# Kernel optimization log

Hardware: AMD Instinct MI355X
Metric: run time of the kernel (lower is better)

Reference implementation:

```python
import jax, jax.numpy as jnp
import numpy as np
from jax import lax

BATCH, SEQ_LEN, INPUT_DIM, OUTPUT_DIM = 64, 1000, 512, 512
KERNEL_WIDTH = 5  # context [-2, 2] with full_context=True -> range(-2, 3)


def setup_inputs() -> dict:
    key = jax.random.key(0)
    k1, k2, k3 = jax.random.split(key, 3)
    stdv = 1.0 / np.sqrt(INPUT_DIM)
    x = jax.random.normal(k1, (BATCH, SEQ_LEN, INPUT_DIM), dtype=jnp.float32)
    kernel = stdv * jax.random.normal(k2, (OUTPUT_DIM, INPUT_DIM, KERNEL_WIDTH), dtype=jnp.float32)
    bias = stdv * jax.random.normal(k3, (OUTPUT_DIM,), dtype=jnp.float32)
    return {"x": x, "kernel": kernel, "bias": bias}


def reference(x, kernel, bias):
    # x: [B, T, C_in] -> [B, C_in, T]
    xt = jnp.transpose(x, (0, 2, 1))
    # Contiguous full context == single VALID conv over time.
    # Original loop: for each valid step i, gather x[:, :, context+i] and conv1d,
    # which for context=range(-2,3) is exactly this strided convolution.
    out = lax.conv_general_dilated(
        xt, kernel,
        window_strides=(1,), padding="VALID",
        dimension_numbers=("NCH", "OIH", "NCH"),
    )  # [B, C_out, T - K + 1]
    out = out + bias[None, :, None]
    # ReLU then transpose back to [B, T_valid, C_out]
    return jnp.transpose(jax.nn.relu(out), (0, 2, 1))
```

## Files before the change

### kernel.cpp

```cpp
#include <hip/hip_runtime.h>
#include <hip/hip_bf16.h>


#define BATCH 64
#define SEQ   1000
#define CIN   512
#define COUT  512
#define TOUT  996
#define KTOT  2560
#define MTOT  63744
#define NKT   40
#define MT    498
#define NT    4
#define NWG   (MT*NT)

typedef __bf16 bf16x8 __attribute__((ext_vector_type(8)));
typedef float  f32x4  __attribute__((ext_vector_type(4)));

__device__ __forceinline__ void gload_lds16(const void* g, void* l) {
  __builtin_amdgcn_global_load_lds(
      (const __attribute__((address_space(1))) void*)g,
      (__attribute__((address_space(3))) void*)l, 16, 0, 0);
}

#define BAR()    __builtin_amdgcn_s_barrier()
#define VM12()   asm volatile("s_waitcnt vmcnt(12)" ::: "memory")
#define VM8()    asm volatile("s_waitcnt vmcnt(8)"  ::: "memory")
#define VM4()    asm volatile("s_waitcnt vmcnt(4)"  ::: "memory")
#define PRIO(x)  __builtin_amdgcn_s_setprio(x)
#define SCHED0() __builtin_amdgcn_sched_barrier(0)
#define MFMA(d, x, y) d = __builtin_amdgcn_mfma_f32_16x16x32_bf16(x, y, d, 0, 0, 0)

__global__ void cvt_x_kernel(const float* __restrict__ x, __bf16* __restrict__ xb, int n) {
  int i = (blockIdx.x * blockDim.x + threadIdx.x) * 8;
  if (i >= n) return;
  float4 f0 = *(const float4*)(x + i);
  float4 f1 = *(const float4*)(x + i + 4);
  bf16x8 v;
  v[0] = (__bf16)f0.x; v[1] = (__bf16)f0.y; v[2] = (__bf16)f0.z; v[3] = (__bf16)f0.w;
  v[4] = (__bf16)f1.x; v[5] = (__bf16)f1.y; v[6] = (__bf16)f1.z; v[7] = (__bf16)f1.w;
  *(bf16x8*)(xb + i) = v;
}

__global__ void cvt_w_kernel(const float* __restrict__ k, __bf16* __restrict__ wt) {
  int idx = blockIdx.x * blockDim.x + threadIdx.x;
  if (idx >= 80 * 32 * 512) return;
  int j  = idx & 7;
  int l  = (idx >> 3) & 63;
  int t1 = idx >> 9;
  int ob = t1 & 31;
  int ks = t1 >> 5;
  int o  = ob * 16 + (l & 15);
  int kk = ks * 32 + ((l >> 4) & 3) * 8 + j;
  int c  = kk & 511, kw = kk >> 9;
  wt[idx] = (__bf16)k[(o * CIN + c) * 5 + kw];
}

#define STAGE(buf, kt) do { \
    char* d_ = (char*)Ab + ((buf) << 14); \
    gload_lds16(Xb + offA0 + (kt) * 64, d_ + dof0); \
    gload_lds16(Xb + offA1 + (kt) * 64, d_ + dof1); \
    gload_lds16(Xb + offA2 + (kt) * 64, d_ + dof2); \
    gload_lds16(Xb + offA3 + (kt) * 64, d_ + dof3); } while (0)

#define LOADB(bn, Tn) do { \
    const char* p_ = Wglob + (size_t)(Tn) * 65536; \
    bn[0][0] = *(const bf16x8*)(p_ +     0); bn[0][1] = *(const bf16x8*)(p_ + 32768); \
    bn[1][0] = *(const bf16x8*)(p_ +  1024); bn[1][1] = *(const bf16x8*)(p_ + 33792); \
    bn[2][0] = *(const bf16x8*)(p_ +  2048); bn[2][1] = *(const bf16x8*)(p_ + 34816); \
    bn[3][0] = *(const bf16x8*)(p_ +  3072); bn[3][1] = *(const bf16x8*)(p_ + 35840); } while (0)

#define TILE(T, bc, bn) do { \
    const bool s1_ = (T) + 1 < NKT, s2_ = (T) + 2 < NKT; \
    if (s1_) LOADB(bn, (T) + 1); \
    if (s2_) STAGE(((T) + 2) & 3, (T) + 2); \
    const char* Ac_ = Aw + (((T) & 3) << 14); \
    bf16x8 a_[4][2]; \
    _Pragma("unroll") \
    for (int mi = 0; mi < 4; ++mi) { \
      a_[mi][0] = *(const bf16x8*)(Ac_ + mi * 2048 + off0); \
      a_[mi][1] = *(const bf16x8*)(Ac_ + mi * 2048 + off1); \
    } \
    PRIO(1); \
    _Pragma("unroll") \
    for (int mi = 0; mi < 4; ++mi) \
      _Pragma("unroll") \
      for (int nj = 0; nj < 4; ++nj) { \
        MFMA(acc[mi][nj], a_[mi][0], bc[nj][0]); \
        MFMA(acc[mi][nj], a_[mi][1], bc[nj][1]); \
      } \
    PRIO(0); \
    SCHED0(); \
    if (s2_) { VM12(); } else if (s1_) { VM8(); } \
    if (s1_) BAR(); \
  } while (0)

__global__ __launch_bounds__(256, 2)
void tdnn_gemm_kernel(const __bf16* __restrict__ Xb, const __bf16* __restrict__ Wt2,
                      const float* __restrict__ bias, float* __restrict__ out) {
  __shared__ __bf16 Ab[4][128][64];

  const int tid  = threadIdx.x;
  const int wave = tid >> 6;
  const int lane = tid & 63;
  const int wr = wave >> 1;
  const int wc = wave & 1;

  int bid = blockIdx.x;
  int swz = (bid & 7) * 249 + (bid >> 3);
  const int m0 = (swz >> 2) * 128;
  const int n0 = (swz & 3) * 128;

  int offA0, offA1, offA2, offA3, dof0, dof1, dof2, dof3;
  {
    int rr, ce, m, b, tt;
#define MKOFF(l, A, D) \
    rr = (l) * 32 + (tid >> 3); \
    ce = (((tid & 7) ^ (rr & 7)) << 3); \
    D  = ((l) * 256 + tid) * 16; \
    m = m0 + rr; b = m / TOUT; tt = m - b * TOUT; \
    A = (b * SEQ + tt) * CIN + ce;
    MKOFF(0, offA0, dof0)
    MKOFF(1, offA1, dof1)
    MKOFF(2, offA2, dof2)
    MKOFF(3, offA3, dof3)
#undef MKOFF
  }

  const int frow = lane & 15;
  const int fkb  = (lane >> 4) << 4;
  const int xorv = (frow & 7) << 4;
  const int off0 = fkb ^ xorv;
  const int off1 = (64 + fkb) ^ xorv;
  const char* Aw = (const char*)Ab + (wr * 64 + frow) * 128;

  const int obW = (n0 >> 4) + wc * 4;
  const char* Wglob = (const char*)Wt2 + obW * 1024 + lane * 16;

  f32x4 acc[4][4];
  const f32x4 z = {0.f, 0.f, 0.f, 0.f};
#pragma unroll
  for (int i = 0; i < 4; i++)
#pragma unroll
    for (int j = 0; j < 4; j++) acc[i][j] = z;

  bf16x8 bA[4][2], bB[4][2];

  LOADB(bA, 0);
  STAGE(0, 0);
  STAGE(1, 1);
  VM4();
  BAR();

  for (int T = 0; T < NKT; T += 2) {
    TILE(T,     bA, bB);
    TILE(T + 1, bB, bA);
  }

  const int ccol = lane & 15;
  const int crow = (lane >> 4) * 4;
  float bv[4];
#pragma unroll
  for (int nj = 0; nj < 4; ++nj)
    bv[nj] = bias[n0 + wc * 64 + nj * 16 + ccol];

#pragma unroll
  for (int mi = 0; mi < 4; ++mi) {
    const int mrow = m0 + wr * 64 + mi * 16 + crow;
#pragma unroll
    for (int nj = 0; nj < 4; ++nj) {
      const int ocol = n0 + wc * 64 + nj * 16 + ccol;
#pragma unroll
      for (int j = 0; j < 4; ++j) {
        float v = acc[mi][nj][j] + bv[nj];
        v = v > 0.f ? v : 0.f;
        out[(size_t)(mrow + j) * COUT + ocol] = v;
      }
    }
  }
}

extern "C" void kernel_launch(void* const* d_in, const int* in_sizes, int n_in,
                              void* d_out, int out_size, void* d_ws, size_t ws_size,
                              hipStream_t stream) {
  const float* x      = (const float*)d_in[0];
  const float* kernel = (const float*)d_in[1];
  const float* bias   = (const float*)d_in[2];
  float* out          = (float*)d_out;

  __bf16* xb  = (__bf16*)d_ws;
  __bf16* wt2 = (__bf16*)((char*)d_ws + (size_t)BATCH * SEQ * CIN * 2);

  const int nx = BATCH * SEQ * CIN;
  cvt_x_kernel<<<nx / 8 / 256, 256, 0, stream>>>(x, xb, nx);
  cvt_w_kernel<<<(80 * 32 * 512 + 255) / 256, 256, 0, stream>>>(kernel, wt2);
  tdnn_gemm_kernel<<<NWG, 256, 0, stream>>>(xb, wt2, bias, out);
}
```

Measured before the change: 201.6 us.

## Fuse fp32-to-bf16 conversion of x into the GEMM A-tile staging

Removes the separate pass that converts x to bf16. The GEMM now loads the fp32 activations into registers, converts them to bf16, and writes them into the swizzled LDS buffers, replacing the direct global-to-LDS loads. This avoids a full extra read and write of the activation tensor. The cost is twice the global bytes per A tile, roughly 32 extra VGPRs, and LDS stores issued by the waves themselves, which may hurt occupancy or overlap.

```diff
diff --git a/kernel.cpp b/kernel.cpp
--- a/kernel.cpp
+++ b/kernel.cpp
@@ -17,30 +17,13 @@
 typedef __bf16 bf16x8 __attribute__((ext_vector_type(8)));
 typedef float  f32x4  __attribute__((ext_vector_type(4)));
 
-__device__ __forceinline__ void gload_lds16(const void* g, void* l) {
-  __builtin_amdgcn_global_load_lds(
-      (const __attribute__((address_space(1))) void*)g,
-      (__attribute__((address_space(3))) void*)l, 16, 0, 0);
-}
-
 #define BAR()    __builtin_amdgcn_s_barrier()
-#define VM12()   asm volatile("s_waitcnt vmcnt(12)" ::: "memory")
 #define VM8()    asm volatile("s_waitcnt vmcnt(8)"  ::: "memory")
-#define VM4()    asm volatile("s_waitcnt vmcnt(4)"  ::: "memory")
+#define VM0()    asm volatile("s_waitcnt vmcnt(0)"  ::: "memory")
+#define LGKM0()  asm volatile("s_waitcnt lgkmcnt(0)" ::: "memory")
 #define PRIO(x)  __builtin_amdgcn_s_setprio(x)
 #define SCHED0() __builtin_amdgcn_sched_barrier(0)
 #define MFMA(d, x, y) d = __builtin_amdgcn_mfma_f32_16x16x32_bf16(x, y, d, 0, 0, 0)
-
-__global__ void cvt_x_kernel(const float* __restrict__ x, __bf16* __restrict__ xb, int n) {
-  int i = (blockIdx.x * blockDim.x + threadIdx.x) * 8;
-  if (i >= n) return;
-  float4 f0 = *(const float4*)(x + i);
-  float4 f1 = *(const float4*)(x + i + 4);
-  bf16x8 v;
-  v[0] = (__bf16)f0.x; v[1] = (__bf16)f0.y; v[2] = (__bf16)f0.z; v[3] = (__bf16)f0.w;
-  v[4] = (__bf16)f1.x; v[5] = (__bf16)f1.y; v[6] = (__bf16)f1.z; v[7] = (__bf16)f1.w;
-  *(bf16x8*)(xb + i) = v;
-}
 
 __global__ void cvt_w_kernel(const float* __restrict__ k, __bf16* __restrict__ wt) {
   int idx = blockIdx.x * blockDim.x + threadIdx.x;
@@ -56,12 +39,23 @@
   wt[idx] = (__bf16)k[(o * CIN + c) * 5 + kw];
 }
 
-#define STAGE(buf, kt) do { \
-    char* d_ = (char*)Ab + ((buf) << 14); \
-    gload_lds16(Xb + offA0 + (kt) * 64, d_ + dof0); \
-    gload_lds16(Xb + offA1 + (kt) * 64, d_ + dof1); \
-    gload_lds16(Xb + offA2 + (kt) * 64, d_ + dof2); \
-    gload_lds16(Xb + offA3 + (kt) * 64, d_ + dof3); } while (0)
+#define LOADA(kt) do { \
+    const float* p_; \
+    p_ = Xf + offA0 + (kt) * 64; fa00 = *(const f32x4*)p_; fa01 = *(const f32x4*)(p_ + 4); \
+    p_ = Xf + offA1 + (kt) * 64; fa10 = *(const f32x4*)p_; fa11 = *(const f32x4*)(p_ + 4); \
+    p_ = Xf + offA2 + (kt) * 64; fa20 = *(const f32x4*)p_; fa21 = *(const f32x4*)(p_ + 4); \
+    p_ = Xf + offA3 + (kt) * 64; fa30 = *(const f32x4*)p_; fa31 = *(const f32x4*)(p_ + 4); } while (0)
+
+#define CVW1(lo, hi, dof, buf) do { \
+    bf16x8 v_; \
+    v_[0] = (__bf16)lo[0]; v_[1] = (__bf16)lo[1]; v_[2] = (__bf16)lo[2]; v_[3] = (__bf16)lo[3]; \
+    v_[4] = (__bf16)hi[0]; v_[5] = (__bf16)hi[1]; v_[6] = (__bf16)hi[2]; v_[7] = (__bf16)hi[3]; \
+    *(bf16x8*)((char*)Ab + ((buf) << 14) + dof) = v_; } while (0)
+#define WRITEA(buf) do { \
+    CVW1(fa00, fa01, dof0, buf); \
+    CVW1(fa10, fa11, dof1, buf); \
+    CVW1(fa20, fa21, dof2, buf); \
+    CVW1(fa30, fa31, dof3, buf); } while (0)
 
 #define LOADB(bn, Tn) do { \
     const char* p_ = Wglob + (size_t)(Tn) * 65536; \
@@ -72,8 +66,8 @@
 
 #define TILE(T, bc, bn) do { \
     const bool s1_ = (T) + 1 < NKT, s2_ = (T) + 2 < NKT; \
+    if (s2_) LOADA((T) + 2); \
     if (s1_) LOADB(bn, (T) + 1); \
-    if (s2_) STAGE(((T) + 2) & 3, (T) + 2); \
     const char* Ac_ = Aw + (((T) & 3) << 14); \
     bf16x8 a_[4][2]; \
     _Pragma("unroll") \
@@ -91,12 +85,12 @@
       } \
     PRIO(0); \
     SCHED0(); \
-    if (s2_) { VM12(); } else if (s1_) { VM8(); } \
+    if (s2_) { VM8(); WRITEA(((T) + 2) & 3); } \
     if (s1_) BAR(); \
   } while (0)
 
 __global__ __launch_bounds__(256, 2)
-void tdnn_gemm_kernel(const __bf16* __restrict__ Xb, const __bf16* __restrict__ Wt2,
+void tdnn_gemm_kernel(const float* __restrict__ Xf, const __bf16* __restrict__ Wt2,
                       const float* __restrict__ bias, float* __restrict__ out) {
   __shared__ __bf16 Ab[4][128][64];
 
@@ -145,11 +139,16 @@
     for (int j = 0; j < 4; j++) acc[i][j] = z;
 
   bf16x8 bA[4][2], bB[4][2];
+  f32x4 fa00, fa01, fa10, fa11, fa20, fa21, fa30, fa31;
 
+  LOADA(0);
   LOADB(bA, 0);
-  STAGE(0, 0);
-  STAGE(1, 1);
-  VM4();
+  VM8();
+  WRITEA(0);
+  LOADA(1);
+  VM0();
+  WRITEA(1);
+  LGKM0();
   BAR();
 
   for (int T = 0; T < NKT; T += 2) {
@@ -188,11 +187,8 @@
   const float* bias   = (const float*)d_in[2];
   float* out          = (float*)d_out;
 
-  __bf16* xb  = (__bf16*)d_ws;
-  __bf16* wt2 = (__bf16*)((char*)d_ws + (size_t)BATCH * SEQ * CIN * 2);
+  __bf16* wt2 = (__bf16*)d_ws;
 
-  const int nx = BATCH * SEQ * CIN;
-  cvt_x_kernel<<<nx / 8 / 256, 256, 0, stream>>>(x, xb, nx);
   cvt_w_kernel<<<(80 * 32 * 512 + 255) / 256, 256, 0, stream>>>(kernel, wt2);
-  tdnn_gemm_kernel<<<NWG, 256, 0, stream>>>(xb, wt2, bias, out);
+  tdnn_gemm_kernel<<<NWG, 256, 0, stream>>>(x, wt2, bias, out);
 }
```

Result: slower. 241.2 us (+19.7%).
